# Kernel optimization log

Measured on AMD Instinct MI355X. Metric: run time of the kernel, lower is better.

The kernel has to match this reference:

```python
import jax, jax.numpy as jnp
import numpy as np

HID = 2048; NH = 16; NKV = 2; HD = 128; G = NH // NKV
SEC = (16, 24, 24)  # sums to 64 = HD/2
EPS = 1e-6
B, S = 2, 1024


def _reorder(table):
    # table: [3, B, S, HD]; interleave sections picking axis i%3 per chunk
    chunks = []
    idx = 0
    for _ in range(2):
        for sec in SEC:
            chunks.append(table[..., idx:idx + sec])
            idx += sec
    return jnp.concatenate([c[i % len(SEC)] for i, c in enumerate(chunks)], axis=-1)  # [B,S,HD]


def rotate_half(x):
    x1, x2 = jnp.split(x, 2, axis=-1)
    return jnp.concatenate((-x2, x1), axis=-1)


def rms_norm(x, gamma):
    var = jnp.mean(jnp.square(x), axis=-1, keepdims=True)
    return gamma * (x * jax.lax.rsqrt(var + EPS))


def setup_inputs() -> dict:
    key = jax.random.key(0)
    ks = jax.random.split(key, 12)
    x = jax.random.normal(ks[0], (B, S, HID), dtype=jnp.float32)
    ang = jax.random.uniform(ks[1], (3, B, S, HD), dtype=jnp.float32) * 6.28318
    cos = jnp.cos(ang)
    sin = jnp.sin(ang)
    mask = jnp.ones((B, S), dtype=jnp.float32)
    sc = 0.02
    q_w = jax.random.normal(ks[2], (HID, NH * HD), dtype=jnp.float32) * sc
    q_b = jnp.zeros((NH * HD,), dtype=jnp.float32)
    k_w = jax.random.normal(ks[3], (HID, NKV * HD), dtype=jnp.float32) * sc
    k_b = jnp.zeros((NKV * HD,), dtype=jnp.float32)
    v_w = jax.random.normal(ks[4], (HID, NKV * HD), dtype=jnp.float32) * sc
    v_b = jnp.zeros((NKV * HD,), dtype=jnp.float32)
    q_gamma = jnp.ones((HD,), dtype=jnp.float32)
    k_gamma = jnp.ones((HD,), dtype=jnp.float32)
    o_w = jax.random.normal(ks[5], (NH * HD, HID), dtype=jnp.float32) * sc
    return {"x": x, "cos": cos, "sin": sin, "mask": mask,
            "q_w": q_w, "q_b": q_b, "k_w": k_w, "k_b": k_b,
            "v_w": v_w, "v_b": v_b, "q_gamma": q_gamma, "k_gamma": k_gamma,
            "o_w": o_w}


def reference(x, cos, sin, mask, q_w, q_b, k_w, k_b, v_w, v_b, q_gamma, k_gamma, o_w):
    b, s, _ = x.shape
    # QKV projections
    q = (x @ q_w + q_b).reshape(b, s, NH, HD)
    k = (x @ k_w + k_b).reshape(b, s, NKV, HD)
    v = (x @ v_w + v_b).reshape(b, s, NKV, HD)
    # per-head RMSNorm on q, k
    q = rms_norm(q, q_gamma)
    k = rms_norm(k, k_gamma)
    q = jnp.transpose(q, (0, 2, 1, 3))  # [B,NH,S,HD]
    k = jnp.transpose(k, (0, 2, 1, 3))  # [B,NKV,S,HD]
    v = jnp.transpose(v, (0, 2, 1, 3))
    # multimodal RoPE
    cos_f = _reorder(cos)[:, None, :, :]  # [B,1,S,HD]
    sin_f = _reorder(sin)[:, None, :, :]
    q = q * cos_f + rotate_half(q) * sin_f
    k = k * cos_f + rotate_half(k) * sin_f
    # key-mask zeroing and effective lengths
    eff = mask.sum(axis=-1).astype(jnp.int32)  # [B]
    bm = mask[:, None, :, None]
    k = k * bm
    v = v * bm
    hist = (jnp.arange(s)[None, :] < eff[:, None]).astype(jnp.float32)  # [B,S]
    # GQA attention scores in fp32
    qg = q.reshape(b, NKV, G, s, HD)
    scores = jnp.einsum('bngqd,bnkd->bngqk', qg, k,
                        precision=jax.lax.Precision.HIGHEST) * (HD ** -0.5)
    scores = scores.reshape(b, NH, s, s)
    scores = scores + (1.0 - hist)[:, None, None, :] * -1e9
    causal = jnp.tril(jnp.ones((s, s), dtype=jnp.float32))
    scores = scores + (1.0 - causal)[None, None, :, :] * -1e9
    aw = jax.nn.softmax(scores, axis=-1)
    # weighted values
    out = jnp.einsum('bngqk,bnkd->bngqd', aw.reshape(b, NKV, G, s, s), v,
                     precision=jax.lax.Precision.HIGHEST)
    out = out.reshape(b, NH, s, HD)
    out = jnp.transpose(out, (0, 2, 1, 3)).reshape(b, s, NH * HD)
    return out @ o_w
```

## Files before the change

kernel.cpp:

```cpp
#include <hip/hip_runtime.h>

typedef __attribute__((ext_vector_type(8))) short bf16x8;
typedef __attribute__((ext_vector_type(4))) float f32x4;

#define MFMA16(a, b, c) __builtin_amdgcn_mfma_f32_16x16x32_bf16(a, b, c, 0, 0, 0)

__device__ inline short f2bf(float f) {
  union { float f; unsigned u; } v;
  v.f = f;
  unsigned r = v.u + 0x7FFF + ((v.u >> 16) & 1);
  return (short)(r >> 16);
}
__device__ inline float bf2f(short s) {
  union { unsigned u; float f; } v;
  v.u = ((unsigned)(unsigned short)s) << 16;
  return v.f;
}
#define GLD_LDS16(g, l)                                                        \
  __builtin_amdgcn_global_load_lds(                                            \
      (const __attribute__((address_space(1))) unsigned int*)(g),              \
      (__attribute__((address_space(3))) unsigned int*)(l), 16, 0, 0)

__device__ __forceinline__ void raw_barrier() {
  __asm__ volatile("" ::: "memory");
  __builtin_amdgcn_s_barrier();
  __asm__ volatile("" ::: "memory");
}

__global__ __launch_bounds__(256) void prep_kernel(
    const float* __restrict__ x, const float* __restrict__ q_w,
    const float* __restrict__ k_w, const float* __restrict__ v_w,
    const float* __restrict__ o_w, short* __restrict__ xb,
    short* __restrict__ wqkv_t, short* __restrict__ wo_t) {
  __shared__ float t[64][65];
  int bid = blockIdx.x;
  if (bid < 4096) {
    int i = (bid * 256 + threadIdx.x) * 4;
    float4 f = *(const float4*)&x[i];
    short4 o;
    o.x = f2bf(f.x); o.y = f2bf(f.y); o.z = f2bf(f.z); o.w = f2bf(f.w);
    *(short4*)&xb[i] = o;
    return;
  }
  bid -= 4096;
  const float* src;
  short* dst;
  int C, bx, by;
  if (bid < 1024) {
    src = q_w; dst = wqkv_t; C = 2048;
    bx = (bid & 31) * 64; by = (bid >> 5) * 64;
  } else if (bid < 1152) {
    bid -= 1024;
    src = k_w; dst = wqkv_t + (size_t)2048 * 2048; C = 256;
    bx = (bid & 3) * 64; by = (bid >> 2) * 64;
  } else if (bid < 1280) {
    bid -= 1152;
    src = v_w; dst = wqkv_t + (size_t)2304 * 2048; C = 256;
    bx = (bid & 3) * 64; by = (bid >> 2) * 64;
  } else {
    bid -= 1280;
    src = o_w; dst = wo_t; C = 2048;
    bx = (bid & 31) * 64; by = (bid >> 5) * 64;
  }
  const int R = 2048;
  const int tx = threadIdx.x & 15;
  const int ty = threadIdx.x >> 4;
#pragma unroll
  for (int i = 0; i < 4; i++) {
    int row = ty + i * 16;
    float4 f = *(const float4*)&src[(size_t)(by + row) * C + bx + tx * 4];
    t[row][tx * 4 + 0] = f.x;
    t[row][tx * 4 + 1] = f.y;
    t[row][tx * 4 + 2] = f.z;
    t[row][tx * 4 + 3] = f.w;
  }
  __syncthreads();
#pragma unroll
  for (int i = 0; i < 4; i++) {
    int c = ty + i * 16;
    short4 o;
    o.x = f2bf(t[tx * 4 + 0][c]);
    o.y = f2bf(t[tx * 4 + 1][c]);
    o.z = f2bf(t[tx * 4 + 2][c]);
    o.w = f2bf(t[tx * 4 + 3][c]);
    *(short4*)&dst[(size_t)(bx + c) * R + by + tx * 4] = o;
  }
}

__global__ __launch_bounds__(256) void gemm_db_kernel(const short* __restrict__ A,
                                                      const short* __restrict__ B,
                                                      float* __restrict__ C, int N) {
  __shared__ __align__(16) short As[4][128 * 32];
  __shared__ __align__(16) short Bs[4][128 * 32];
  const int tid = threadIdx.x;
  const int lane = tid & 63, wave = tid >> 6;
  const int quad = lane >> 4, l16 = lane & 15;
  const int m0 = blockIdx.y * 128, n0 = blockIdx.x * 128;
  const int wm = (wave >> 1) * 64, wn = (wave & 1) * 64;
  const int r0 = tid >> 2, c0 = (tid & 3) * 8;
  const size_t arow0 = (size_t)(m0 + r0) * 2048, arow1 = (size_t)(m0 + r0 + 64) * 2048;
  const size_t brow0 = (size_t)(n0 + r0) * 2048, brow1 = (size_t)(n0 + r0 + 64) * 2048;
  f32x4 acc[4][4];
#pragma unroll
  for (int mi = 0; mi < 4; mi++)
#pragma unroll
    for (int ni = 0; ni < 4; ni++) acc[mi][ni] = (f32x4){0.f, 0.f, 0.f, 0.f};

#pragma unroll
  for (int st = 0; st < 3; st++) {
    const int kk = st * 32 + c0;
    GLD_LDS16(&A[arow0 + kk], &As[st][r0 * 32 + c0]);
    GLD_LDS16(&A[arow1 + kk], &As[st][(r0 + 64) * 32 + c0]);
    GLD_LDS16(&B[brow0 + kk], &Bs[st][r0 * 32 + c0]);
    GLD_LDS16(&B[brow1 + kk], &Bs[st][(r0 + 64) * 32 + c0]);
  }

  for (int ki = 0; ki < 64; ki++) {
    const int cur = ki & 3;
    if (ki < 61) {
      const int nxt = (ki + 3) & 3;
      const int kk = (ki + 3) * 32 + c0;
      GLD_LDS16(&A[arow0 + kk], &As[nxt][r0 * 32 + c0]);
      GLD_LDS16(&A[arow1 + kk], &As[nxt][(r0 + 64) * 32 + c0]);
      GLD_LDS16(&B[brow0 + kk], &Bs[nxt][r0 * 32 + c0]);
      GLD_LDS16(&B[brow1 + kk], &Bs[nxt][(r0 + 64) * 32 + c0]);
      __asm__ volatile("s_waitcnt vmcnt(12)" ::: "memory");
    } else if (ki == 61) {
      __asm__ volatile("s_waitcnt vmcnt(8)" ::: "memory");
    } else if (ki == 62) {
      __asm__ volatile("s_waitcnt vmcnt(4)" ::: "memory");
    } else {
      __asm__ volatile("s_waitcnt vmcnt(0)" ::: "memory");
    }
    raw_barrier();
    bf16x8 af[4], bfr[4];
#pragma unroll
    for (int mi = 0; mi < 4; mi++)
      af[mi] = *(const bf16x8*)&As[cur][(wm + mi * 16 + l16) * 32 + quad * 8];
#pragma unroll
    for (int ni = 0; ni < 4; ni++)
      bfr[ni] = *(const bf16x8*)&Bs[cur][(wn + ni * 16 + l16) * 32 + quad * 8];
#pragma unroll
    for (int mi = 0; mi < 4; mi++)
#pragma unroll
      for (int ni = 0; ni < 4; ni++)
        acc[mi][ni] = MFMA16(af[mi], bfr[ni], acc[mi][ni]);
    __asm__ volatile("s_waitcnt lgkmcnt(0)" ::: "memory");
    raw_barrier();
  }
#pragma unroll
  for (int mi = 0; mi < 4; mi++)
#pragma unroll
    for (int ni = 0; ni < 4; ni++)
#pragma unroll
      for (int r = 0; r < 4; r++)
        C[(size_t)(m0 + wm + mi * 16 + quad * 4 + r) * N + n0 + wn + ni * 16 + l16] =
            acc[mi][ni][r];
}

__global__ __launch_bounds__(256) void qkv_post_kernel(
    const float* __restrict__ qkv, const float* __restrict__ qbias,
    const float* __restrict__ kbias, const float* __restrict__ qg,
    const float* __restrict__ kg, const float* __restrict__ cosb,
    const float* __restrict__ sinb, const float* __restrict__ maskp,
    short* __restrict__ qo, short* __restrict__ ko) {
  const int rid = blockIdx.x * 4 + (threadIdx.x >> 6);
  const int lane = threadIdx.x & 63;
  const int slot = rid >> 11;
  const int bs = rid & 2047;
  const int b = bs >> 10, s = bs & 1023;
  const float* row = qkv + (size_t)bs * 2560;
  int off;
  const float* bias;
  const float* gamma;
  if (slot < 16) { off = slot * 128; bias = qbias + slot * 128; gamma = qg; }
  else { off = 2048 + (slot - 16) * 128; bias = kbias + (slot - 16) * 128; gamma = kg; }
  float v0 = row[off + lane] + bias[lane];
  float v1 = row[off + 64 + lane] + bias[64 + lane];
  float ss = v0 * v0 + v1 * v1;
#pragma unroll
  for (int o = 1; o < 64; o <<= 1) ss += __shfl_xor(ss, o);
  float r = rsqrtf(ss * (1.0f / 128.0f) + 1e-6f);
  v0 = gamma[lane] * v0 * r;
  v1 = gamma[64 + lane] * v1 * r;
  int sel = (lane < 16) ? 0 : (lane < 40) ? 1 : 2;
  size_t ci = ((size_t)(sel * 2 + b) * 1024 + s) * 128 + lane;
  float c0 = cosb[ci], s0 = sinb[ci], c1 = cosb[ci + 64], s1 = sinb[ci + 64];
  float o0 = v0 * c0 - v1 * s0;
  float o1 = v1 * c1 + v0 * s1;
  if (slot >= 16) { float mk = maskp[bs]; o0 *= mk; o1 *= mk; }
  size_t oidx;
  short* optr;
  if (slot < 16) { oidx = (((size_t)(b * 16 + slot) * 1024) + s) * 128; optr = qo; }
  else { oidx = (((size_t)(b * 2 + (slot - 16)) * 1024) + s) * 128; optr = ko; }
  optr[oidx + lane] = f2bf(o0);
  optr[oidx + 64 + lane] = f2bf(o1);
}

__global__ __launch_bounds__(256) void vtrans_kernel(const float* __restrict__ qkv,
                                                     const float* __restrict__ vbias,
                                                     const float* __restrict__ maskp,
                                                     short* __restrict__ vtb) {
  __shared__ short t[32][33];
  const int bz = blockIdx.z;
  const int bq = bz >> 1, kv = bz & 1;
  const int d0 = blockIdx.x * 32, s0 = blockIdx.y * 32;
  const int tx = threadIdx.x & 31;
  const int ty = threadIdx.x >> 5;
#pragma unroll
  for (int i = 0; i < 4; i++) {
    int s = s0 + ty + i * 8;
    float val = qkv[((size_t)(bq * 1024 + s)) * 2560 + 2304 + kv * 128 + d0 + tx] +
                vbias[kv * 128 + d0 + tx];
    t[ty + i * 8][tx] = f2bf(val * maskp[bq * 1024 + s]);
  }
  __syncthreads();
#pragma unroll
  for (int i = 0; i < 4; i++)
    vtb[((size_t)bz * 128 + d0 + ty + i * 8) * 1024 + s0 + tx] = t[tx][ty + i * 8];
}

__global__ __launch_bounds__(256) void attn_kernel(const short* __restrict__ Q,
                                                   const short* __restrict__ K,
                                                   const short* __restrict__ Vt_g,
                                                   short* __restrict__ po,
                                                   float* __restrict__ pml) {
  int x = blockIdx.x;
  const int h = blockIdx.y;
  const int b = blockIdx.z;
  int g = 0, base = 0;
  while (x >= base + 4 * (g + 1)) { base += 4 * (g + 1); g++; }
  const int r0 = x - base;
  const int qt = 4 * g + r0 / (g + 1);
  const int kc = r0 % (g + 1);
  int nsteps = qt - 4 * kc + 1;
  if (nsteps > 4) nsteps = 4;

  const int kv = h >> 3;
  const int tid = threadIdx.x;
  const int wave = tid >> 6, lane = tid & 63;
  const int quad = lane >> 4, l16 = lane & 15;
  __shared__ __align__(16) short Ks[64 * 136];
  __shared__ __align__(16) short Vs[128 * 72];
  __shared__ __align__(16) short Ps[4][16 * 68];

  const size_t qoff = (((size_t)(b * 16 + h) * 1024) + qt * 64 + wave * 16 + l16) * 128;
  bf16x8 aq[4];
#pragma unroll
  for (int kk = 0; kk < 4; kk++) aq[kk] = *(const bf16x8*)&Q[qoff + kk * 32 + quad * 8];

  f32x4 o[8];
#pragma unroll
  for (int i = 0; i < 8; i++) o[i] = (f32x4){0.f, 0.f, 0.f, 0.f};
  float m[4], l[4];
#pragma unroll
  for (int r = 0; r < 4; r++) { m[r] = -1e30f; l[r] = 0.f; }
  const int qrow0 = qt * 64 + wave * 16 + quad * 4;
  const size_t koff = ((size_t)(b * 2 + kv) * 1024) * 128;
  const size_t voff = koff;
  const float scale = 0.08838834764831845f;

  for (int st = 0; st < nsteps; st++) {
    const int ks0 = kc * 256 + st * 64;
#pragma unroll
    for (int it = 0; it < 4; it++) {
      int c = it * 256 + tid;
      {
        int row = c >> 4, cc = (c & 15) * 8;
        *(int4*)&Ks[row * 136 + cc] =
            *(const int4*)&K[koff + (size_t)(ks0 + row) * 128 + cc];
      }
      {
        int d = c >> 3, cc = (c & 7) * 8;
        *(int4*)&Vs[d * 72 + cc] =
            *(const int4*)&Vt_g[voff + (size_t)d * 1024 + ks0 + cc];
      }
    }
    __syncthreads();
    f32x4 sc[4];
#pragma unroll
    for (int nt = 0; nt < 4; nt++) sc[nt] = (f32x4){0.f, 0.f, 0.f, 0.f};
#pragma unroll
    for (int nt = 0; nt < 4; nt++)
#pragma unroll
      for (int kk = 0; kk < 4; kk++) {
        bf16x8 bk = *(const bf16x8*)&Ks[(nt * 16 + l16) * 136 + kk * 32 + quad * 8];
        sc[nt] = MFMA16(aq[kk], bk, sc[nt]);
      }
    float sv[4][4], mx[4];
#pragma unroll
    for (int r = 0; r < 4; r++) mx[r] = -1e30f;
#pragma unroll
    for (int nt = 0; nt < 4; nt++)
#pragma unroll
      for (int r = 0; r < 4; r++) {
        float s = sc[nt][r] * scale;
        int kcol = ks0 + nt * 16 + l16;
        if (kcol > qrow0 + r) s = -1e30f;
        sv[nt][r] = s;
        mx[r] = fmaxf(mx[r], s);
      }
#pragma unroll
    for (int off = 1; off < 16; off <<= 1)
#pragma unroll
      for (int r = 0; r < 4; r++) mx[r] = fmaxf(mx[r], __shfl_xor(mx[r], off));
    float alpha[4];
#pragma unroll
    for (int r = 0; r < 4; r++) {
      float mn = fmaxf(m[r], mx[r]);
      alpha[r] = __expf(m[r] - mn);
      m[r] = mn;
    }
    float rs[4] = {0.f, 0.f, 0.f, 0.f};
#pragma unroll
    for (int nt = 0; nt < 4; nt++)
#pragma unroll
      for (int r = 0; r < 4; r++) {
        float p = __expf(sv[nt][r] - m[r]);
        sv[nt][r] = p;
        rs[r] += p;
      }
#pragma unroll
    for (int r = 0; r < 4; r++) l[r] = l[r] * alpha[r] + rs[r];
#pragma unroll
    for (int i = 0; i < 8; i++)
#pragma unroll
      for (int r = 0; r < 4; r++) o[i][r] *= alpha[r];
    short* P = &Ps[wave][0];
#pragma unroll
    for (int nt = 0; nt < 4; nt++)
#pragma unroll
      for (int r = 0; r < 4; r++)
        P[(quad * 4 + r) * 68 + nt * 16 + l16] = f2bf(sv[nt][r]);
    __asm__ volatile("s_waitcnt lgkmcnt(0)" ::: "memory");
    bf16x8 pa0 = *(const bf16x8*)&P[l16 * 68 + quad * 8];
    bf16x8 pa1 = *(const bf16x8*)&P[l16 * 68 + 32 + quad * 8];
#pragma unroll
    for (int nt = 0; nt < 8; nt++) {
      bf16x8 bv0 = *(const bf16x8*)&Vs[(nt * 16 + l16) * 72 + quad * 8];
      bf16x8 bv1 = *(const bf16x8*)&Vs[(nt * 16 + l16) * 72 + 32 + quad * 8];
      o[nt] = MFMA16(pa0, bv0, o[nt]);
      o[nt] = MFMA16(pa1, bv1, o[nt]);
    }
    __syncthreads();
  }
#pragma unroll
  for (int off = 1; off < 16; off <<= 1)
#pragma unroll
    for (int r = 0; r < 4; r++) l[r] += __shfl_xor(l[r], off);
  const int p = (b * 16 + h) * 40 + blockIdx.x;
  const int lrow = wave * 16 + quad * 4;
#pragma unroll
  for (int nt = 0; nt < 8; nt++)
#pragma unroll
    for (int r = 0; r < 4; r++)
      po[(size_t)p * 8192 + (size_t)(lrow + r) * 128 + nt * 16 + l16] = f2bf(o[nt][r]);
  if (l16 == 0) {
#pragma unroll
    for (int r = 0; r < 4; r++) {
      pml[(size_t)p * 128 + lrow + r] = m[r];
      pml[(size_t)p * 128 + 64 + lrow + r] = l[r];
    }
  }
}

__global__ __launch_bounds__(256) void attn_combine_kernel(const short* __restrict__ po,
                                                           const float* __restrict__ pml,
                                                           short* __restrict__ attn) {
  const int qt = blockIdx.x, h = blockIdx.y, b = blockIdx.z;
  const int g = qt >> 2, nc = g + 1;
  const int x0 = 2 * g * (g + 1) + (qt & 3) * nc;
  const int row = threadIdx.x >> 2;
  const int d0 = (threadIdx.x & 3) * 32;
  const int pbase = (b * 16 + h) * 40 + x0;
  float mm[4], ll[4], M = -1e30f;
#pragma unroll
  for (int kc = 0; kc < 4; kc++)
    if (kc < nc) {
      mm[kc] = pml[(size_t)(pbase + kc) * 128 + row];
      ll[kc] = pml[(size_t)(pbase + kc) * 128 + 64 + row];
      M = fmaxf(M, mm[kc]);
    }
  float denom = 0.f, sc[4];
#pragma unroll
  for (int kc = 0; kc < 4; kc++)
    if (kc < nc) { sc[kc] = __expf(mm[kc] - M); denom += sc[kc] * ll[kc]; }
  float inv = 1.f / denom;
  float acc[32];
#pragma unroll
  for (int j = 0; j < 32; j++) acc[j] = 0.f;
#pragma unroll
  for (int kc = 0; kc < 4; kc++)
    if (kc < nc) {
      const short* src = po + (size_t)(pbase + kc) * 8192 + (size_t)row * 128 + d0;
#pragma unroll
      for (int j = 0; j < 4; j++) {
        int4 v = *(const int4*)&src[j * 8];
        const short* vs = (const short*)&v;
#pragma unroll
        for (int e = 0; e < 8; e++) acc[j * 8 + e] += sc[kc] * bf2f(vs[e]);
      }
    }
  short ob[32];
#pragma unroll
  for (int j = 0; j < 32; j++) ob[j] = f2bf(acc[j] * inv);
  short* dst = attn + ((size_t)(b * 1024 + qt * 64 + row)) * 2048 + h * 128 + d0;
#pragma unroll
  for (int j = 0; j < 4; j++) *(int4*)&dst[j * 8] = *(const int4*)&ob[j * 8];
}

extern "C" void kernel_launch(void* const* d_in, const int* in_sizes, int n_in,
                              void* d_out, int out_size, void* d_ws, size_t ws_size,
                              hipStream_t stream) {
  const float* x = (const float*)d_in[0];
  const float* cosb = (const float*)d_in[1];
  const float* sinb = (const float*)d_in[2];
  const float* mask = (const float*)d_in[3];
  const float* q_w = (const float*)d_in[4];
  const float* q_b = (const float*)d_in[5];
  const float* k_w = (const float*)d_in[6];
  const float* k_b = (const float*)d_in[7];
  const float* v_w = (const float*)d_in[8];
  const float* v_b = (const float*)d_in[9];
  const float* qg = (const float*)d_in[10];
  const float* kg = (const float*)d_in[11];
  const float* o_w = (const float*)d_in[12];
  float* out = (float*)d_out;

  char* ws = (char*)d_ws;
  short* wo_t = (short*)(ws);
  short* wqkv_t = (short*)(ws + ((size_t)8 << 20));
  float* pml = (float*)(ws + ((size_t)8 << 20));
  short* attn = (short*)(ws + ((size_t)9 << 20));
  short* xb = (short*)(ws + ((size_t)18 << 20));
  short* qb = xb;
  float* qkv_raw = (float*)(ws + ((size_t)26 << 20));
  short* po = (short*)(ws + ((size_t)26 << 20));
  short* kb = (short*)(ws + ((size_t)46 << 20));
  short* vtb = (short*)(ws + ((size_t)47 << 20));

  prep_kernel<<<6400, 256, 0, stream>>>(x, q_w, k_w, v_w, o_w, xb, wqkv_t, wo_t);
  gemm_db_kernel<<<dim3(20, 16), 256, 0, stream>>>(xb, wqkv_t, qkv_raw, 2560);
  qkv_post_kernel<<<9216, 256, 0, stream>>>(qkv_raw, q_b, k_b, qg, kg, cosb, sinb, mask,
                                            qb, kb);
  vtrans_kernel<<<dim3(4, 32, 4), 256, 0, stream>>>(qkv_raw, v_b, mask, vtb);
  attn_kernel<<<dim3(40, 16, 2), 256, 0, stream>>>(qb, kb, vtb, po, pml);
  attn_combine_kernel<<<dim3(16, 16, 2), 256, 0, stream>>>(po, pml, attn);
  gemm_db_kernel<<<dim3(16, 16), 256, 0, stream>>>(attn, wo_t, out, 2048);
}
```

Baseline: 263.7 us.

## Process two K-stages per barrier in GEMM and merge QKV post and V-transpose kernels

The GEMM main loop now handles two 32-wide K stages per iteration, so barriers and waitcnts happen half as often. Loads for the next two stages are issued after the second barrier, with 4 stages prefetched up front. Separately, the q/k norm+RoPE kernel and the V transpose kernel are merged into one launch that dispatches on block index, saving one kernel launch. The trade-off is a shallower effective prefetch distance: the next loads start only after compute, which can expose memory latency.

```diff
diff --git a/kernel.cpp b/kernel.cpp
--- a/kernel.cpp
+++ b/kernel.cpp
@@ -107,7 +107,7 @@
     for (int ni = 0; ni < 4; ni++) acc[mi][ni] = (f32x4){0.f, 0.f, 0.f, 0.f};
 
 #pragma unroll
-  for (int st = 0; st < 3; st++) {
+  for (int st = 0; st < 4; st++) {
     const int kk = st * 32 + c0;
     GLD_LDS16(&A[arow0 + kk], &As[st][r0 * 32 + c0]);
     GLD_LDS16(&A[arow1 + kk], &As[st][(r0 + 64) * 32 + c0]);
@@ -115,38 +115,43 @@
     GLD_LDS16(&B[brow1 + kk], &Bs[st][(r0 + 64) * 32 + c0]);
   }
 
-  for (int ki = 0; ki < 64; ki++) {
-    const int cur = ki & 3;
-    if (ki < 61) {
-      const int nxt = (ki + 3) & 3;
-      const int kk = (ki + 3) * 32 + c0;
-      GLD_LDS16(&A[arow0 + kk], &As[nxt][r0 * 32 + c0]);
-      GLD_LDS16(&A[arow1 + kk], &As[nxt][(r0 + 64) * 32 + c0]);
-      GLD_LDS16(&B[brow0 + kk], &Bs[nxt][r0 * 32 + c0]);
-      GLD_LDS16(&B[brow1 + kk], &Bs[nxt][(r0 + 64) * 32 + c0]);
-      __asm__ volatile("s_waitcnt vmcnt(12)" ::: "memory");
-    } else if (ki == 61) {
+  for (int p = 0; p < 32; p++) {
+    if (p < 31) {
       __asm__ volatile("s_waitcnt vmcnt(8)" ::: "memory");
-    } else if (ki == 62) {
-      __asm__ volatile("s_waitcnt vmcnt(4)" ::: "memory");
     } else {
       __asm__ volatile("s_waitcnt vmcnt(0)" ::: "memory");
     }
     raw_barrier();
-    bf16x8 af[4], bfr[4];
-#pragma unroll
-    for (int mi = 0; mi < 4; mi++)
-      af[mi] = *(const bf16x8*)&As[cur][(wm + mi * 16 + l16) * 32 + quad * 8];
-#pragma unroll
-    for (int ni = 0; ni < 4; ni++)
-      bfr[ni] = *(const bf16x8*)&Bs[cur][(wn + ni * 16 + l16) * 32 + quad * 8];
-#pragma unroll
-    for (int mi = 0; mi < 4; mi++)
+#pragma unroll
+    for (int j = 0; j < 2; j++) {
+      const int cur = (2 * p + j) & 3;
+      bf16x8 af[4], bfr[4];
+#pragma unroll
+      for (int mi = 0; mi < 4; mi++)
+        af[mi] = *(const bf16x8*)&As[cur][(wm + mi * 16 + l16) * 32 + quad * 8];
 #pragma unroll
       for (int ni = 0; ni < 4; ni++)
-        acc[mi][ni] = MFMA16(af[mi], bfr[ni], acc[mi][ni]);
+        bfr[ni] = *(const bf16x8*)&Bs[cur][(wn + ni * 16 + l16) * 32 + quad * 8];
+#pragma unroll
+      for (int mi = 0; mi < 4; mi++)
+#pragma unroll
+        for (int ni = 0; ni < 4; ni++)
+          acc[mi][ni] = MFMA16(af[mi], bfr[ni], acc[mi][ni]);
+    }
     __asm__ volatile("s_waitcnt lgkmcnt(0)" ::: "memory");
     raw_barrier();
+    if (p < 30) {
+#pragma unroll
+      for (int j = 0; j < 2; j++) {
+        const int st = 2 * p + 4 + j;
+        const int slot = st & 3;
+        const int kk = st * 32 + c0;
+        GLD_LDS16(&A[arow0 + kk], &As[slot][r0 * 32 + c0]);
+        GLD_LDS16(&A[arow1 + kk], &As[slot][(r0 + 64) * 32 + c0]);
+        GLD_LDS16(&B[brow0 + kk], &Bs[slot][r0 * 32 + c0]);
+        GLD_LDS16(&B[brow1 + kk], &Bs[slot][(r0 + 64) * 32 + c0]);
+      }
+    }
   }
 #pragma unroll
   for (int mi = 0; mi < 4; mi++)
@@ -158,53 +163,54 @@
             acc[mi][ni][r];
 }
 
-__global__ __launch_bounds__(256) void qkv_post_kernel(
+__global__ __launch_bounds__(256) void postv_kernel(
     const float* __restrict__ qkv, const float* __restrict__ qbias,
-    const float* __restrict__ kbias, const float* __restrict__ qg,
-    const float* __restrict__ kg, const float* __restrict__ cosb,
-    const float* __restrict__ sinb, const float* __restrict__ maskp,
-    short* __restrict__ qo, short* __restrict__ ko) {
-  const int rid = blockIdx.x * 4 + (threadIdx.x >> 6);
-  const int lane = threadIdx.x & 63;
-  const int slot = rid >> 11;
-  const int bs = rid & 2047;
-  const int b = bs >> 10, s = bs & 1023;
-  const float* row = qkv + (size_t)bs * 2560;
-  int off;
-  const float* bias;
-  const float* gamma;
-  if (slot < 16) { off = slot * 128; bias = qbias + slot * 128; gamma = qg; }
-  else { off = 2048 + (slot - 16) * 128; bias = kbias + (slot - 16) * 128; gamma = kg; }
-  float v0 = row[off + lane] + bias[lane];
-  float v1 = row[off + 64 + lane] + bias[64 + lane];
-  float ss = v0 * v0 + v1 * v1;
-#pragma unroll
-  for (int o = 1; o < 64; o <<= 1) ss += __shfl_xor(ss, o);
-  float r = rsqrtf(ss * (1.0f / 128.0f) + 1e-6f);
-  v0 = gamma[lane] * v0 * r;
-  v1 = gamma[64 + lane] * v1 * r;
-  int sel = (lane < 16) ? 0 : (lane < 40) ? 1 : 2;
-  size_t ci = ((size_t)(sel * 2 + b) * 1024 + s) * 128 + lane;
-  float c0 = cosb[ci], s0 = sinb[ci], c1 = cosb[ci + 64], s1 = sinb[ci + 64];
-  float o0 = v0 * c0 - v1 * s0;
-  float o1 = v1 * c1 + v0 * s1;
-  if (slot >= 16) { float mk = maskp[bs]; o0 *= mk; o1 *= mk; }
-  size_t oidx;
-  short* optr;
-  if (slot < 16) { oidx = (((size_t)(b * 16 + slot) * 1024) + s) * 128; optr = qo; }
-  else { oidx = (((size_t)(b * 2 + (slot - 16)) * 1024) + s) * 128; optr = ko; }
-  optr[oidx + lane] = f2bf(o0);
-  optr[oidx + 64 + lane] = f2bf(o1);
-}
-
-__global__ __launch_bounds__(256) void vtrans_kernel(const float* __restrict__ qkv,
-                                                     const float* __restrict__ vbias,
-                                                     const float* __restrict__ maskp,
-                                                     short* __restrict__ vtb) {
+    const float* __restrict__ kbias, const float* __restrict__ vbias,
+    const float* __restrict__ qg, const float* __restrict__ kg,
+    const float* __restrict__ cosb, const float* __restrict__ sinb,
+    const float* __restrict__ maskp, short* __restrict__ qo, short* __restrict__ ko,
+    short* __restrict__ vtb) {
   __shared__ short t[32][33];
-  const int bz = blockIdx.z;
+  const int bid = blockIdx.x;
+  if (bid < 9216) {
+    const int rid = bid * 4 + (threadIdx.x >> 6);
+    const int lane = threadIdx.x & 63;
+    const int slot = rid >> 11;
+    const int bs = rid & 2047;
+    const int b = bs >> 10, s = bs & 1023;
+    const float* row = qkv + (size_t)bs * 2560;
+    int off;
+    const float* bias;
+    const float* gamma;
+    if (slot < 16) { off = slot * 128; bias = qbias + slot * 128; gamma = qg; }
+    else { off = 2048 + (slot - 16) * 128; bias = kbias + (slot - 16) * 128; gamma = kg; }
+    float v0 = row[off + lane] + bias[lane];
+    float v1 = row[off + 64 + lane] + bias[64 + lane];
+    float ss = v0 * v0 + v1 * v1;
+#pragma unroll
+    for (int o = 1; o < 64; o <<= 1) ss += __shfl_xor(ss, o);
+    float r = rsqrtf(ss * (1.0f / 128.0f) + 1e-6f);
+    v0 = gamma[lane] * v0 * r;
+    v1 = gamma[64 + lane] * v1 * r;
+    int sel = (lane < 16) ? 0 : (lane < 40) ? 1 : 2;
+    size_t ci = ((size_t)(sel * 2 + b) * 1024 + s) * 128 + lane;
+    float c0 = cosb[ci], s0 = sinb[ci], c1 = cosb[ci + 64], s1 = sinb[ci + 64];
+    float o0 = v0 * c0 - v1 * s0;
+    float o1 = v1 * c1 + v0 * s1;
+    if (slot >= 16) { float mk = maskp[bs]; o0 *= mk; o1 *= mk; }
+    size_t oidx;
+    short* optr;
+    if (slot < 16) { oidx = (((size_t)(b * 16 + slot) * 1024) + s) * 128; optr = qo; }
+    else { oidx = (((size_t)(b * 2 + (slot - 16)) * 1024) + s) * 128; optr = ko; }
+    optr[oidx + lane] = f2bf(o0);
+    optr[oidx + 64 + lane] = f2bf(o1);
+    return;
+  }
+  const int b2 = bid - 9216;
+  const int d0 = (b2 & 3) * 32;
+  const int s0 = ((b2 >> 2) & 31) * 32;
+  const int bz = b2 >> 7;
   const int bq = bz >> 1, kv = bz & 1;
-  const int d0 = blockIdx.x * 32, s0 = blockIdx.y * 32;
   const int tx = threadIdx.x & 31;
   const int ty = threadIdx.x >> 5;
 #pragma unroll
@@ -441,9 +447,8 @@
 
   prep_kernel<<<6400, 256, 0, stream>>>(x, q_w, k_w, v_w, o_w, xb, wqkv_t, wo_t);
   gemm_db_kernel<<<dim3(20, 16), 256, 0, stream>>>(xb, wqkv_t, qkv_raw, 2560);
-  qkv_post_kernel<<<9216, 256, 0, stream>>>(qkv_raw, q_b, k_b, qg, kg, cosb, sinb, mask,
-                                            qb, kb);
-  vtrans_kernel<<<dim3(4, 32, 4), 256, 0, stream>>>(qkv_raw, v_b, mask, vtb);
+  postv_kernel<<<9728, 256, 0, stream>>>(qkv_raw, q_b, k_b, v_b, qg, kg, cosb, sinb, mask,
+                                         qb, kb, vtb);
   attn_kernel<<<dim3(40, 16, 2), 256, 0, stream>>>(qb, kb, vtb, po, pml);
   attn_combine_kernel<<<dim3(16, 16, 2), 256, 0, stream>>>(po, pml, attn);
   gemm_db_kernel<<<dim3(16, 16), 256, 0, stream>>>(attn, wo_t, out, 2048);
```

Result: faster. 253.3 us (-4.0%).
